# Optimization experiments

Measured on AMD Instinct MI355X. Metric: run time of the kernel, lower is better.

## Reference

```python
import jax, jax.numpy as jnp
import numpy as np

T = 1.0  # temperature (default in original forward)


def setup_inputs() -> dict:
    key = jax.random.key(0)
    k1, k2 = jax.random.split(key)
    N, M, D = 65536, 512, 256
    z = jax.random.normal(k1, (N, D), dtype=jnp.float32)
    e = jax.random.normal(k2, (M, D), dtype=jnp.float32)
    log_sigma = jnp.zeros((1,), dtype=jnp.float32)  # init_log_sigma = 0.0
    return {"z": z, "e": e, "log_sigma": log_sigma}


def reference(z, e, log_sigma):
    N, z_dim = z.shape
    M = e.shape[0]
    # pad N up to a multiple of M (zeros), then view as [B, M, z_dim]
    N_pad = ((N + M - 1) // M) * M
    z = jnp.pad(z, ((0, N_pad - N), (0, 0)))
    zb = z.reshape(-1, M, z_dim)  # [B, M, D]
    # squared euclidean distance via GEMM form: ||z||^2 + ||e||^2 - 2 z.e -> [B, M, M]
    dist = (
        jnp.sum(zb * zb, axis=-1)[:, :, None]
        + jnp.sum(e * e, axis=-1)[None, None, :]
        - 2.0 * jnp.einsum("bmd,kd->bmk", zb, e)
    )
    alpha = -1.0 / (2.0 * jnp.exp(log_sigma[0]) ** 2)
    # logsumexp over the z-block dim (axis=1), mean over codebook dim (axis=1 after reduce)
    loss = -jnp.mean(T * jax.nn.logsumexp(alpha * dist / T, axis=1), axis=1)  # [B]
    loss = loss + 0.5 * z_dim * (2.0 * log_sigma[0] - 1.0) + jnp.log(jnp.float32(M))
    return jnp.mean(loss)
```

## Files before the change

### kernel.cpp

```cpp
#include <hip/hip_runtime.h>
#include <stdint.h>
#include <math.h>

typedef __attribute__((ext_vector_type(8))) short short8;
typedef __attribute__((ext_vector_type(4))) float f32x4;

#define DEVI static __device__ __forceinline__

constexpr int D = 256;

constexpr size_t WS_EIMG  = 0;
constexpr size_t WS_ETERM = 262144;
constexpr size_t WS_WMAX  = 264192;
constexpr size_t WS_WSUM  = WS_WMAX + 2097152;
constexpr size_t WS_PART  = WS_WSUM + 2097152;

DEVI unsigned int f2bf(float f) {
  unsigned int u = __float_as_uint(f);
  return (u + 0x7fffu + ((u >> 16) & 1u)) >> 16;
}
DEVI float shflx(float v, int m) { return __shfl_xor(v, m, 64); }

__global__ void prep_e(const float* __restrict__ e, const float* __restrict__ lsp,
                       char* __restrict__ eimg, float* __restrict__ eterm) {
  const int et = blockIdx.x, t = threadIdx.x;
  const int c = t >> 3, o = t & 7;
  const int gc = et * 32 + c;
  const float a = __expf(-2.0f * lsp[0]);
  const float* s = e + (size_t)gc * D + o * 32;
  float sq = 0.0f;
  unsigned int w[16];
#pragma unroll
  for (int i = 0; i < 8; ++i) {
    float4 x = *(const float4*)(s + i * 4);
    sq += x.x * x.x + x.y * x.y + x.z * x.z + x.w * x.w;
    w[2 * i]     = f2bf(a * x.x) | (f2bf(a * x.y) << 16);
    w[2 * i + 1] = f2bf(a * x.z) | (f2bf(a * x.w) << 16);
  }
  sq += shflx(sq, 1); sq += shflx(sq, 2); sq += shflx(sq, 4);
  char* base = eimg + (size_t)et * 16384;
#pragma unroll
  for (int g = 0; g < 4; ++g) {
    int k2 = o * 4 + g;
    int phys = (c * 512 + k2 * 16) ^ ((c & 7) << 4);
    uint4 pk; pk.x = w[4 * g]; pk.y = w[4 * g + 1];
    pk.z = w[4 * g + 2]; pk.w = w[4 * g + 3];
    *(uint4*)(base + phys) = pk;
  }
  if (o == 0) eterm[gc] = -0.5f * a * sq;
}

__global__ __launch_bounds__(256, 4)
void lse_main(const float* __restrict__ z, const char* __restrict__ eimg,
              const float* __restrict__ lsp, float* __restrict__ wmax,
              float* __restrict__ wsum) {
  __shared__ char  ebuf[2][16384];
  __shared__ float zterm[64];
  __shared__ float pmaxb[2][4][32];
  __shared__ float psumb[2][4][32];

  const int tid = threadIdx.x;
  const int wid = tid >> 6, lane = tid & 63;
  const int r16 = lane & 15;
  const int q   = lane >> 4;
  const int bx = blockIdx.x;
  const float a = __expf(-2.0f * lsp[0]);

  uint4 er[4];
#pragma unroll
  for (int i = 0; i < 4; ++i)
    er[i] = *(const uint4*)(eimg + i * 4096 + tid * 16);

  short8 A[8];
  const float* zs = z + ((size_t)bx * 64 + wid * 16 + r16) * D + q * 8;
  float sq = 0.0f;
#pragma unroll
  for (int g4 = 0; g4 < 4; ++g4) {
#pragma unroll
    for (int s2 = 0; s2 < 2; ++s2) {
      const int s = g4 * 2 + s2;
      float4 x0 = *(const float4*)(zs + s * 32);
      float4 x1 = *(const float4*)(zs + s * 32 + 4);
      sq += x0.x * x0.x + x0.y * x0.y + x0.z * x0.z + x0.w * x0.w +
            x1.x * x1.x + x1.y * x1.y + x1.z * x1.z + x1.w * x1.w;
      uint4 pk;
      pk.x = f2bf(x0.x) | (f2bf(x0.y) << 16);
      pk.y = f2bf(x0.z) | (f2bf(x0.w) << 16);
      pk.z = f2bf(x1.x) | (f2bf(x1.y) << 16);
      pk.w = f2bf(x1.z) | (f2bf(x1.w) << 16);
      A[s] = __builtin_bit_cast(short8, pk);
    }
    asm volatile("" ::: "memory");
  }
  sq += shflx(sq, 16); sq += shflx(sq, 32);
  if (q == 0) zterm[wid * 16 + r16] = -0.5f * a * sq;

#pragma unroll
  for (int i = 0; i < 4; ++i)
    *(uint4*)(&ebuf[0][0] + i * 4096 + tid * 16) = er[i];
  __syncthreads();

  for (int p = 0; p < 16; ++p) {
    const int cur = p & 1;
    if (p < 15) {
#pragma unroll
      for (int i = 0; i < 4; ++i)
        er[i] = *(const uint4*)(eimg + (size_t)(p + 1) * 16384 + i * 4096 + tid * 16);
    }

    f32x4 acc0 = {0.f, 0.f, 0.f, 0.f}, acc1 = {0.f, 0.f, 0.f, 0.f};
    const char* bp = &ebuf[cur][0];
#pragma unroll
    for (int s = 0; s < 8; ++s) {
      const int phys = (r16 * 512 + s * 64 + q * 16) ^ ((lane & 7) << 4);
      short8 B0 = *(const short8*)(bp + phys);
      short8 B1 = *(const short8*)(bp + phys + 8192);
      acc0 = __builtin_amdgcn_mfma_f32_16x16x32_bf16(A[s], B0, acc0, 0, 0, 0);
      acc1 = __builtin_amdgcn_mfma_f32_16x16x32_bf16(A[s], B1, acc1, 0, 0, 0);
    }

    float zt[4], v0[4], v1[4];
#pragma unroll
    for (int j = 0; j < 4; ++j) zt[j] = zterm[wid * 16 + q * 4 + j];
#pragma unroll
    for (int j = 0; j < 4; ++j) { v0[j] = acc0[j] + zt[j]; v1[j] = acc1[j] + zt[j]; }
    float mx0 = fmaxf(fmaxf(v0[0], v0[1]), fmaxf(v0[2], v0[3]));
    float mx1 = fmaxf(fmaxf(v1[0], v1[1]), fmaxf(v1[2], v1[3]));
    mx0 = fmaxf(mx0, shflx(mx0, 16)); mx0 = fmaxf(mx0, shflx(mx0, 32));
    mx1 = fmaxf(mx1, shflx(mx1, 16)); mx1 = fmaxf(mx1, shflx(mx1, 32));
    float sm0 = __expf(v0[0] - mx0) + __expf(v0[1] - mx0) +
                __expf(v0[2] - mx0) + __expf(v0[3] - mx0);
    float sm1 = __expf(v1[0] - mx1) + __expf(v1[1] - mx1) +
                __expf(v1[2] - mx1) + __expf(v1[3] - mx1);
    sm0 += shflx(sm0, 16); sm0 += shflx(sm0, 32);
    sm1 += shflx(sm1, 16); sm1 += shflx(sm1, 32);
    if (q == 0) {
      pmaxb[cur][wid][r16] = mx0;      psumb[cur][wid][r16] = sm0;
      pmaxb[cur][wid][16 + r16] = mx1; psumb[cur][wid][16 + r16] = sm1;
    }
    if (p < 15) {
#pragma unroll
      for (int i = 0; i < 4; ++i)
        *(uint4*)(&ebuf[cur ^ 1][0] + i * 4096 + tid * 16) = er[i];
    }
    __syncthreads();

    if (tid < 32) {
      float m0 = pmaxb[cur][0][tid], m1 = pmaxb[cur][1][tid];
      float m2 = pmaxb[cur][2][tid], m3 = pmaxb[cur][3][tid];
      float nm = fmaxf(fmaxf(m0, m1), fmaxf(m2, m3));
      float s = psumb[cur][0][tid] * __expf(m0 - nm) +
                psumb[cur][1][tid] * __expf(m1 - nm) +
                psumb[cur][2][tid] * __expf(m2 - nm) +
                psumb[cur][3][tid] * __expf(m3 - nm);
      wmax[(size_t)bx * 512 + p * 32 + tid] = nm;
      wsum[(size_t)bx * 512 + p * 32 + tid] = s;
    }
  }
}

__global__ void merge_b(const float* __restrict__ wmax, const float* __restrict__ wsum,
                        const float* __restrict__ eterm, float* __restrict__ partial) {
  __shared__ float sh[512];
  const int b = blockIdx.x, t = threadIdx.x;
  float m[8];
  float nm = -1e30f;
#pragma unroll
  for (int i = 0; i < 8; ++i) {
    m[i] = wmax[(size_t)(8 * b + i) * 512 + t];
    nm = fmaxf(nm, m[i]);
  }
  float s = 0.0f;
#pragma unroll
  for (int i = 0; i < 8; ++i)
    s += wsum[(size_t)(8 * b + i) * 512 + t] * __expf(m[i] - nm);
  sh[t] = nm + logf(s) + eterm[t];
  __syncthreads();
  for (int st = 256; st > 0; st >>= 1) {
    if (t < st) sh[t] += sh[t + st];
    __syncthreads();
  }
  if (t == 0) partial[b] = sh[0];
}

__global__ void final_k(const float* __restrict__ partial,
                        const float* __restrict__ lsp, float* __restrict__ out) {
  __shared__ float sh[128];
  const int t = threadIdx.x;
  sh[t] = partial[t];
  __syncthreads();
  for (int st = 64; st > 0; st >>= 1) {
    if (t < st) sh[t] += sh[t + st];
    __syncthreads();
  }
  if (t == 0) {
    float ls = lsp[0];
    out[0] = -sh[0] / 65536.0f + 128.0f * (2.0f * ls - 1.0f) + logf(512.0f);
  }
}

extern "C" void kernel_launch(void* const* d_in, const int* in_sizes, int n_in,
                              void* d_out, int out_size, void* d_ws, size_t ws_size,
                              hipStream_t stream) {
  const float* z   = (const float*)d_in[0];
  const float* e   = (const float*)d_in[1];
  const float* lsp = (const float*)d_in[2];
  float* out = (float*)d_out;
  char* ws = (char*)d_ws;
  char*  eimg    = ws + WS_EIMG;
  float* eterm   = (float*)(ws + WS_ETERM);
  float* wmax    = (float*)(ws + WS_WMAX);
  float* wsum    = (float*)(ws + WS_WSUM);
  float* partial = (float*)(ws + WS_PART);

  prep_e<<<dim3(16), dim3(256), 0, stream>>>(e, lsp, eimg, eterm);
  lse_main<<<dim3(1024), dim3(256), 0, stream>>>(z, eimg, lsp, wmax, wsum);
  merge_b<<<dim3(128), dim3(512), 0, stream>>>(wmax, wsum, eterm, partial);
  final_k<<<dim3(1), dim3(128), 0, stream>>>(partial, lsp, out);
}
```

Baseline: 53.70 us.

## Switch main kernel to 32x32x16 MFMA with 128 z rows per block

Each wave now covers 32 z rows with a 32x32x16 bf16 MFMA instead of two 16x16x32 MFMAs over 16 rows, so each block handles 128 rows and the grid is halved. Every codebook tile staged in LDS is therefore reused across twice as many z rows, cutting eimg reloads and per-block sync and reduction overhead. The zterm values are hoisted out of the p loop and the cross-lane reductions shrink to a single xor-32 shuffle. In exchange register use rises (16 A fragments and a 16-wide accumulator), occupancy bounds drop to 2, and there are only 512 blocks to spread across the CUs.

```diff
diff --git a/kernel.cpp b/kernel.cpp
--- a/kernel.cpp
+++ b/kernel.cpp
@@ -3,7 +3,7 @@
 #include <math.h>
 
 typedef __attribute__((ext_vector_type(8))) short short8;
-typedef __attribute__((ext_vector_type(4))) float f32x4;
+typedef __attribute__((ext_vector_type(16))) float f32x16;
 
 #define DEVI static __device__ __forceinline__
 
@@ -12,8 +12,8 @@
 constexpr size_t WS_EIMG  = 0;
 constexpr size_t WS_ETERM = 262144;
 constexpr size_t WS_WMAX  = 264192;
-constexpr size_t WS_WSUM  = WS_WMAX + 2097152;
-constexpr size_t WS_PART  = WS_WSUM + 2097152;
+constexpr size_t WS_WSUM  = WS_WMAX + 1048576;
+constexpr size_t WS_PART  = WS_WSUM + 1048576;
 
 DEVI unsigned int f2bf(float f) {
   unsigned int u = __float_as_uint(f);
@@ -50,19 +50,19 @@
   if (o == 0) eterm[gc] = -0.5f * a * sq;
 }
 
-__global__ __launch_bounds__(256, 4)
+__global__ __launch_bounds__(256, 2)
 void lse_main(const float* __restrict__ z, const char* __restrict__ eimg,
               const float* __restrict__ lsp, float* __restrict__ wmax,
               float* __restrict__ wsum) {
   __shared__ char  ebuf[2][16384];
-  __shared__ float zterm[64];
+  __shared__ float zterm[128];
   __shared__ float pmaxb[2][4][32];
   __shared__ float psumb[2][4][32];
 
   const int tid = threadIdx.x;
   const int wid = tid >> 6, lane = tid & 63;
-  const int r16 = lane & 15;
-  const int q   = lane >> 4;
+  const int l31 = lane & 31;
+  const int hi  = lane >> 5;
   const int bx = blockIdx.x;
   const float a = __expf(-2.0f * lsp[0]);
 
@@ -71,16 +71,16 @@
   for (int i = 0; i < 4; ++i)
     er[i] = *(const uint4*)(eimg + i * 4096 + tid * 16);
 
-  short8 A[8];
-  const float* zs = z + ((size_t)bx * 64 + wid * 16 + r16) * D + q * 8;
+  short8 A[16];
+  const float* zs = z + ((size_t)bx * 128 + wid * 32 + l31) * D + hi * 8;
   float sq = 0.0f;
 #pragma unroll
-  for (int g4 = 0; g4 < 4; ++g4) {
+  for (int g = 0; g < 8; ++g) {
 #pragma unroll
     for (int s2 = 0; s2 < 2; ++s2) {
-      const int s = g4 * 2 + s2;
-      float4 x0 = *(const float4*)(zs + s * 32);
-      float4 x1 = *(const float4*)(zs + s * 32 + 4);
+      const int s = g * 2 + s2;
+      float4 x0 = *(const float4*)(zs + s * 16);
+      float4 x1 = *(const float4*)(zs + s * 16 + 4);
       sq += x0.x * x0.x + x0.y * x0.y + x0.z * x0.z + x0.w * x0.w +
             x1.x * x1.x + x1.y * x1.y + x1.z * x1.z + x1.w * x1.w;
       uint4 pk;
@@ -92,14 +92,22 @@
     }
     asm volatile("" ::: "memory");
   }
-  sq += shflx(sq, 16); sq += shflx(sq, 32);
-  if (q == 0) zterm[wid * 16 + r16] = -0.5f * a * sq;
+  sq += shflx(sq, 32);
+  if (hi == 0) zterm[wid * 32 + l31] = -0.5f * a * sq;
 
 #pragma unroll
   for (int i = 0; i < 4; ++i)
     *(uint4*)(&ebuf[0][0] + i * 4096 + tid * 16) = er[i];
   __syncthreads();
 
+  float zt[16];
+#pragma unroll
+  for (int r = 0; r < 16; ++r)
+    zt[r] = zterm[wid * 32 + (r & 3) + 8 * (r >> 2) + 4 * hi];
+
+  const int cbase = l31 * 512;
+  const int key = (l31 & 7) << 4;
+
   for (int p = 0; p < 16; ++p) {
     const int cur = p & 1;
     if (p < 15) {
@@ -108,35 +116,30 @@
         er[i] = *(const uint4*)(eimg + (size_t)(p + 1) * 16384 + i * 4096 + tid * 16);
     }
 
-    f32x4 acc0 = {0.f, 0.f, 0.f, 0.f}, acc1 = {0.f, 0.f, 0.f, 0.f};
+    f32x16 acc;
+#pragma unroll
+    for (int i = 0; i < 16; ++i) acc[i] = 0.0f;
     const char* bp = &ebuf[cur][0];
 #pragma unroll
-    for (int s = 0; s < 8; ++s) {
-      const int phys = (r16 * 512 + s * 64 + q * 16) ^ ((lane & 7) << 4);
-      short8 B0 = *(const short8*)(bp + phys);
-      short8 B1 = *(const short8*)(bp + phys + 8192);
-      acc0 = __builtin_amdgcn_mfma_f32_16x16x32_bf16(A[s], B0, acc0, 0, 0, 0);
-      acc1 = __builtin_amdgcn_mfma_f32_16x16x32_bf16(A[s], B1, acc1, 0, 0, 0);
-    }
-
-    float zt[4], v0[4], v1[4];
-#pragma unroll
-    for (int j = 0; j < 4; ++j) zt[j] = zterm[wid * 16 + q * 4 + j];
-#pragma unroll
-    for (int j = 0; j < 4; ++j) { v0[j] = acc0[j] + zt[j]; v1[j] = acc1[j] + zt[j]; }
-    float mx0 = fmaxf(fmaxf(v0[0], v0[1]), fmaxf(v0[2], v0[3]));
-    float mx1 = fmaxf(fmaxf(v1[0], v1[1]), fmaxf(v1[2], v1[3]));
-    mx0 = fmaxf(mx0, shflx(mx0, 16)); mx0 = fmaxf(mx0, shflx(mx0, 32));
-    mx1 = fmaxf(mx1, shflx(mx1, 16)); mx1 = fmaxf(mx1, shflx(mx1, 32));
-    float sm0 = __expf(v0[0] - mx0) + __expf(v0[1] - mx0) +
-                __expf(v0[2] - mx0) + __expf(v0[3] - mx0);
-    float sm1 = __expf(v1[0] - mx1) + __expf(v1[1] - mx1) +
-                __expf(v1[2] - mx1) + __expf(v1[3] - mx1);
-    sm0 += shflx(sm0, 16); sm0 += shflx(sm0, 32);
-    sm1 += shflx(sm1, 16); sm1 += shflx(sm1, 32);
-    if (q == 0) {
-      pmaxb[cur][wid][r16] = mx0;      psumb[cur][wid][r16] = sm0;
-      pmaxb[cur][wid][16 + r16] = mx1; psumb[cur][wid][16 + r16] = sm1;
+    for (int s = 0; s < 16; ++s) {
+      short8 B = *(const short8*)(bp + cbase + (((2 * s + hi) * 16) ^ key));
+      acc = __builtin_amdgcn_mfma_f32_32x32x16_bf16(A[s], B, acc, 0, 0, 0);
+    }
+
+    float mx = -1e30f;
+#pragma unroll
+    for (int r = 0; r < 16; ++r) {
+      acc[r] += zt[r];
+      mx = fmaxf(mx, acc[r]);
+    }
+    mx = fmaxf(mx, shflx(mx, 32));
+    float sme = 0.0f;
+#pragma unroll
+    for (int r = 0; r < 16; ++r) sme += __expf(acc[r] - mx);
+    sme += shflx(sme, 32);
+    if (hi == 0) {
+      pmaxb[cur][wid][l31] = mx;
+      psumb[cur][wid][l31] = sme;
     }
     if (p < 15) {
 #pragma unroll
@@ -163,17 +166,17 @@
                         const float* __restrict__ eterm, float* __restrict__ partial) {
   __shared__ float sh[512];
   const int b = blockIdx.x, t = threadIdx.x;
-  float m[8];
+  float m[4];
   float nm = -1e30f;
 #pragma unroll
-  for (int i = 0; i < 8; ++i) {
-    m[i] = wmax[(size_t)(8 * b + i) * 512 + t];
+  for (int i = 0; i < 4; ++i) {
+    m[i] = wmax[(size_t)(4 * b + i) * 512 + t];
     nm = fmaxf(nm, m[i]);
   }
   float s = 0.0f;
 #pragma unroll
-  for (int i = 0; i < 8; ++i)
-    s += wsum[(size_t)(8 * b + i) * 512 + t] * __expf(m[i] - nm);
+  for (int i = 0; i < 4; ++i)
+    s += wsum[(size_t)(4 * b + i) * 512 + t] * __expf(m[i] - nm);
   sh[t] = nm + logf(s) + eterm[t];
   __syncthreads();
   for (int st = 256; st > 0; st >>= 1) {
@@ -214,7 +217,7 @@
   float* partial = (float*)(ws + WS_PART);
 
   prep_e<<<dim3(16), dim3(256), 0, stream>>>(e, lsp, eimg, eterm);
-  lse_main<<<dim3(1024), dim3(256), 0, stream>>>(z, eimg, lsp, wmax, wsum);
+  lse_main<<<dim3(512), dim3(256), 0, stream>>>(z, eimg, lsp, wmax, wsum);
   merge_b<<<dim3(128), dim3(512), 0, stream>>>(wmax, wsum, eterm, partial);
   final_k<<<dim3(1), dim3(128), 0, stream>>>(partial, lsp, out);
 }
```

Measured after the change: 45.49 us. 1.18x faster.
